# Kernel optimization log

Hardware: AMD Instinct MI355X
Metric: run time of the kernel (lower is better)

## Reference

```python
import jax, jax.numpy as jnp
import numpy as np

B, L, D_MODEL, N_HEADS = 2, 2048, 1024, 16
RANK = max(N_HEADS, int(D_MODEL * 0.25))            # 256
RANK_PER_HEAD = RANK // N_HEADS                      # 16
HEAD_DIM = D_MODEL // N_HEADS                        # 64


def _rope_cos_sin(L, head_dim, dtype=jnp.float32):
    half = head_dim // 2
    theta = 1.0 / (10000.0 ** (jnp.arange(half, dtype=dtype) / half))
    angles = jnp.arange(L, dtype=dtype)[:, None] * theta[None, :]   # [L, half]
    return jnp.cos(angles), jnp.sin(angles)


def _apply_rope(x, cos, sin):
    # x: [B, L, H, D]; pairs (even, odd) rotated by per-position angle.
    B, L, H, D = x.shape
    xp = x.reshape(B, L, H, D // 2, 2)
    x0, x1 = xp[..., 0], xp[..., 1]
    c = cos[None, :, None, :]
    s = sin[None, :, None, :]
    r0 = x0 * c - x1 * s
    r1 = x0 * s + x1 * c
    return jnp.stack([r0, r1], axis=-1).reshape(B, L, H, D)


def setup_inputs() -> dict:
    key = jax.random.key(0)
    ks = jax.random.split(key, 7)
    x = jax.random.normal(ks[0], (B, L, D_MODEL), dtype=jnp.float32)
    mask = jax.random.randint(ks[1], (B, L), 0, 2, dtype=jnp.int32)
    scale = 0.02
    Wq = jax.random.normal(ks[2], (RANK, D_MODEL), dtype=jnp.float32) * scale
    Wk = jax.random.normal(ks[3], (RANK, D_MODEL), dtype=jnp.float32) * scale
    Wv = jax.random.normal(ks[4], (RANK, D_MODEL), dtype=jnp.float32) * scale
    xav_u = float(np.sqrt(6.0 / (HEAD_DIM + RANK_PER_HEAD)))
    U = jax.random.uniform(ks[5], (N_HEADS, HEAD_DIM, RANK_PER_HEAD), dtype=jnp.float32, minval=-xav_u, maxval=xav_u)
    V = jax.random.uniform(ks[6], (N_HEADS, RANK_PER_HEAD, HEAD_DIM), dtype=jnp.float32, minval=-xav_u, maxval=xav_u)
    return {"x": x, "Wq": Wq, "Wk": Wk, "Wv": Wv, "U": U, "V": V, "mask": mask}


def reference(x, Wq, Wk, Wv, U, V, mask):
    Bq, Lq, _ = x.shape
    H, HD, RH = U.shape
    q_low = (x @ Wq.T).reshape(Bq, Lq, H, RH)
    k_low = (x @ Wk.T).reshape(Bq, Lq, H, RH)
    v_low = (x @ Wv.T).reshape(Bq, Lq, H, RH)
    # up-project q/k to head_dim via shared U
    q = jnp.einsum('hdr,blhr->blhd', U, q_low)
    k = jnp.einsum('hdr,blhr->blhd', U, k_low)
    cos, sin = _rope_cos_sin(Lq, HD, x.dtype)
    q = _apply_rope(q, cos, sin)
    k = _apply_rope(k, cos, sin)
    attn = jnp.einsum('blhd,bmhd->bhlm', q, k) / jnp.sqrt(jnp.asarray(HD, x.dtype))
    key_mask = mask.astype(bool)[:, None, None, :]           # [B,1,1,M]
    attn = jnp.where(key_mask, attn, jnp.asarray(-jnp.inf, attn.dtype))
    attn = jax.nn.softmax(attn, axis=-1)
    out = jnp.einsum('bhlm,bmhr->blhr', attn, v_low)
    out = jnp.einsum('blhr,hrd->blhd', out, V)
    return out.reshape(Bq, Lq, H * HD)
```

## Files before the change

kernel.cpp:

```cpp
#include <hip/hip_runtime.h>
#include <hip/hip_bf16.h>

typedef unsigned short u16;
typedef unsigned int u32;
typedef __bf16 bf16x8 __attribute__((ext_vector_type(8)));
typedef float f32x4 __attribute__((ext_vector_type(4)));

#define NB 2
#define NL 2048
#define NDM 1024
#define NH 16
#define NHD 64
#define NRH 16
#define NCOL 2304

#define QSCL 0.18033688011112042f

#define AS1(p) ((const __attribute__((address_space(1))) void*)(p))
#define AS3(p) ((__attribute__((address_space(3))) void*)(p))

__device__ __forceinline__ u16 f2bf(float f) {
  u32 u = __builtin_bit_cast(u32, f);
  u32 r = (u + 0x7fffu + ((u >> 16) & 1u)) >> 16;
  return (u16)r;
}

__global__ void k_prep_weff(const float* __restrict__ Wq, const float* __restrict__ Wk,
                            const float* __restrict__ Wv, const float* __restrict__ U,
                            u16* __restrict__ Wall) {
  int idx = blockIdx.x * 256 + threadIdx.x;
  int col = idx & 1023;
  int row = idx >> 10;
  float acc;
  if (row < 2048) {
    const float* W = (row < 1024) ? Wq : Wk;
    int rr = row & 1023;
    int h = rr >> 6, d = rr & 63;
    const float* Uh = U + (h * NHD + d) * NRH;
    const float* Wr = W + (size_t)(h * NRH) * NDM + col;
    acc = 0.f;
#pragma unroll
    for (int r = 0; r < 16; ++r) acc += Uh[r] * Wr[(size_t)r * NDM];
  } else {
    acc = Wv[(size_t)(row - 2048) * NDM + col];
  }
  Wall[idx] = f2bf(acc);
}

__global__ void k_cast_x(const float* __restrict__ x, u16* __restrict__ xb) {
  int i = blockIdx.x * 256 + threadIdx.x;
  float2 v = *(const float2*)(x + (size_t)i * 2);
  ushort2 o;
  o.x = f2bf(v.x);
  o.y = f2bf(v.y);
  *(ushort2*)(xb + (size_t)i * 2) = o;
}

__global__ void k_cstab(float2* __restrict__ cstab) {
  int i = blockIdx.x * 256 + threadIdx.x;
  if (i >= NL * 32) return;
  int l = i >> 5, j = i & 31;
  float theta = 1.0f / powf(10000.0f, (float)j * (1.0f / 32.0f));
  float ang = (float)l * theta;
  cstab[i] = float2{cosf(ang), sinf(ang)};
}

__global__ void k_fbias(const int* __restrict__ mask, float* __restrict__ fb) {
  int i = blockIdx.x * 256 + threadIdx.x;
  fb[i] = mask[i] ? 0.f : -1e30f;
}

__global__ __launch_bounds__(256) void k_gemm(const u16* __restrict__ A,
                                              const u16* __restrict__ Bm,
                                              const float2* __restrict__ cstab,
                                              u16* __restrict__ qt,
                                              u16* __restrict__ ktb,
                                              u16* __restrict__ vT) {
  __shared__ char lds[32768];
  const int tid = threadIdx.x;
  const int wave = tid >> 6, lane = tid & 63;
  const int bm = blockIdx.x, bn = blockIdx.y;
  const int wr = wave >> 1, wc = wave & 1;
  const char* Ag = (const char*)(A + (size_t)bm * 128 * NDM);
  const char* Bg = (const char*)(Bm + (size_t)bn * 128 * NDM);
  f32x4 acc[4][4] = {};
  for (int kt = 0; kt < 16; ++kt) {
    __syncthreads();
#pragma unroll
    for (int i = 0; i < 4; ++i) {
      int off = wave * 4096 + i * 1024 + lane * 16;
      int src = off ^ ((off >> 3) & 0x70);
      int ga = (src >> 7) * 2048 + kt * 128 + (src & 127);
      __builtin_amdgcn_global_load_lds(AS1(Ag + ga), AS3(lds + wave * 4096 + i * 1024), 16, 0, 0);
      __builtin_amdgcn_global_load_lds(AS1(Bg + ga), AS3(lds + 16384 + wave * 4096 + i * 1024), 16, 0, 0);
    }
    __syncthreads();
#pragma unroll
    for (int kk = 0; kk < 2; ++kk) {
      bf16x8 af[4], bfr[4];
#pragma unroll
      for (int m = 0; m < 4; ++m) {
        int row = wr * 64 + m * 16 + (lane & 15);
        int byte = row * 128 + kk * 64 + ((lane >> 4) << 4);
        af[m] = *(const bf16x8*)(lds + (byte ^ ((row & 7) << 4)));
      }
#pragma unroll
      for (int n = 0; n < 4; ++n) {
        int row = wc * 64 + n * 16 + (lane & 15);
        int byte = row * 128 + kk * 64 + ((lane >> 4) << 4);
        bfr[n] = *(const bf16x8*)(lds + 16384 + (byte ^ ((row & 7) << 4)));
      }
#pragma unroll
      for (int m = 0; m < 4; ++m)
#pragma unroll
        for (int n = 0; n < 4; ++n)
          acc[m][n] = __builtin_amdgcn_mfma_f32_16x16x32_bf16(af[m], bfr[n], acc[m][n], 0, 0, 0);
    }
  }

  const int r0 = bm * 128 + wr * 64;
  const int b = r0 >> 11;
  if (bn < 16) {
    const bool isq = (bn < 8);
    u16* dst = isq ? qt : ktb;
    const float qs = isq ? QSCL : 1.0f;
    const int hh = (isq ? bn : bn - 8) * 2 + wc;
    const int par = lane & 1;
    const size_t base = ((size_t)(b * NH + hh)) * NL;
#pragma unroll
    for (int n = 0; n < 4; ++n) {
      const int d = n * 16 + (lane & 15);
      const int j = d >> 1;
#pragma unroll
      for (int m = 0; m < 4; ++m) {
#pragma unroll
        for (int r = 0; r < 4; ++r) {
          int row = r0 + m * 16 + ((lane >> 4) << 2) + r;
          int l = row & 2047;
          float2 cs = cstab[l * 32 + j];
          float v = acc[m][n][r];
          float pv = __shfl_xor(v, 1);
          float ov = par ? (pv * cs.y + v * cs.x) : (v * cs.x - pv * cs.y);
          dst[((base + l) << 6) + d] = f2bf(ov * qs);
        }
      }
    }
  } else {
    const int rr = lane & 15;
#pragma unroll
    for (int n = 0; n < 4; ++n) {
      const int hh = (bn - 16) * 8 + wc * 4 + n;
      const size_t vbase = ((size_t)(b * NH + hh) * NRH + rr) * NL;
#pragma unroll
      for (int m = 0; m < 4; ++m) {
        int row0 = r0 + m * 16 + ((lane >> 4) << 2);
        int l = row0 & 2047;
        int l6 = l & 63;
        int P = (l & ~63) | (((l6 >> 4) & 1) << 5) | (((l6 >> 5) & 1) << 2) |
                (((l6 >> 2) & 3) << 3) | (l6 & 3);
        ushort4 o4;
        o4.x = f2bf(acc[m][n][0]);
        o4.y = f2bf(acc[m][n][1]);
        o4.z = f2bf(acc[m][n][2]);
        o4.w = f2bf(acc[m][n][3]);
        *(ushort4*)(vT + vbase + P) = o4;
      }
    }
  }
}

__global__ __launch_bounds__(256) void k_attn(const u16* __restrict__ qt,
                                              const u16* __restrict__ ktp,
                                              const u16* __restrict__ vT,
                                              const float* __restrict__ fbias,
                                              float* __restrict__ Oattn) {
  __shared__ char lds[16384];
  const int tid = threadIdx.x, wave = tid >> 6, lane = tid & 63;
  int blk = (int)blockIdx.x;
  blk = (blk & 7) * 128 + (blk >> 3);
  const int qtile = blk & 31, h = (blk >> 5) & 15, b = blk >> 9;
  const size_t bh = (size_t)(b * NH + h);
  const u16* Q = qt + (bh * NL + (size_t)qtile * 64) * 64;
  const u16* K = ktp + bh * NL * 64;
  const u16* Vt = vT + bh * NRH * NL;
  const float* fbb = fbias + b * NL;

  const int g = lane >> 4, qi = lane & 15;
  const int swq = (qi & 7) << 4;

  const int qr = wave * 16 + qi;
  bf16x8 qf0 = *(const bf16x8*)(Q + qr * 64 + g * 8);
  bf16x8 qf1 = *(const bf16x8*)(Q + qr * 64 + 32 + g * 8);

  f32x4 o = {0.f, 0.f, 0.f, 0.f};
  float Ls = 0.f;

  const u16* Vrow = Vt + (size_t)qi * NL + g * 8;
  const float* fbg = fbb + g * 4;
  int koff[4][2];
#pragma unroll
  for (int n = 0; n < 4; ++n)
#pragma unroll
    for (int dc = 0; dc < 2; ++dc)
      koff[n][dc] = (((n * 16 + qi) * 128 + dc * 64 + g * 16) ^ swq);

#pragma unroll
  for (int i = 0; i < 2; ++i) {
    int off = wave * 2048 + i * 1024 + lane * 16;
    int src = off ^ ((off >> 3) & 0x70);
    __builtin_amdgcn_global_load_lds(AS1((const char*)K + src),
                                     AS3(lds + wave * 2048 + i * 1024), 16, 0, 0);
  }
  f32x4 cfb0 = *(const f32x4*)(fbg);
  f32x4 cfb1 = *(const f32x4*)(fbg + 16);
  f32x4 cfb2 = *(const f32x4*)(fbg + 32);
  f32x4 cfb3 = *(const f32x4*)(fbg + 48);
  bf16x8 cvf0 = *(const bf16x8*)(Vrow);
  bf16x8 cvf1 = *(const bf16x8*)(Vrow + 32);

  int cur = 0;
  for (int t = 0; t < 32; ++t) {
    __syncthreads();
    f32x4 nfb0 = {}, nfb1 = {}, nfb2 = {}, nfb3 = {};
    bf16x8 nvf0 = {}, nvf1 = {};
    if (t < 31) {
      const char* Kg = (const char*)(K + (size_t)(t + 1) * 4096);
      char* Kn = lds + (cur ^ 1) * 8192;
#pragma unroll
      for (int i = 0; i < 2; ++i) {
        int off = wave * 2048 + i * 1024 + lane * 16;
        int src = off ^ ((off >> 3) & 0x70);
        __builtin_amdgcn_global_load_lds(AS1(Kg + src),
                                         AS3(Kn + wave * 2048 + i * 1024), 16, 0, 0);
      }
      const float* fbt = fbg + (t + 1) * 64;
      nfb0 = *(const f32x4*)(fbt);
      nfb1 = *(const f32x4*)(fbt + 16);
      nfb2 = *(const f32x4*)(fbt + 32);
      nfb3 = *(const f32x4*)(fbt + 48);
      const u16* Vtt = Vrow + (t + 1) * 64;
      nvf0 = *(const bf16x8*)(Vtt);
      nvf1 = *(const bf16x8*)(Vtt + 32);
    }
    const char* Kcur = lds + cur * 8192;

    f32x4 s0, s1, s2, s3;
#define QK(n, dst, fbv)                                                    \
  {                                                                        \
    bf16x8 k0 = *(const bf16x8*)(Kcur + koff[n][0]);                       \
    bf16x8 k1 = *(const bf16x8*)(Kcur + koff[n][1]);                       \
    f32x4 z = __builtin_amdgcn_mfma_f32_16x16x32_bf16(k0, qf0, fbv, 0, 0, 0); \
    dst = __builtin_amdgcn_mfma_f32_16x16x32_bf16(k1, qf1, z, 0, 0, 0);    \
  }
    QK(0, s0, cfb0) QK(1, s1, cfb1) QK(2, s2, cfb2) QK(3, s3, cfb3)
#undef QK

    float p00 = __builtin_amdgcn_exp2f(s0[0]), p01 = __builtin_amdgcn_exp2f(s0[1]);
    float p02 = __builtin_amdgcn_exp2f(s0[2]), p03 = __builtin_amdgcn_exp2f(s0[3]);
    float p10 = __builtin_amdgcn_exp2f(s1[0]), p11 = __builtin_amdgcn_exp2f(s1[1]);
    float p12 = __builtin_amdgcn_exp2f(s1[2]), p13 = __builtin_amdgcn_exp2f(s1[3]);
    float p20 = __builtin_amdgcn_exp2f(s2[0]), p21 = __builtin_amdgcn_exp2f(s2[1]);
    float p22 = __builtin_amdgcn_exp2f(s2[2]), p23 = __builtin_amdgcn_exp2f(s2[3]);
    float p30 = __builtin_amdgcn_exp2f(s3[0]), p31 = __builtin_amdgcn_exp2f(s3[1]);
    float p32 = __builtin_amdgcn_exp2f(s3[2]), p33 = __builtin_amdgcn_exp2f(s3[3]);
    float rs = (((p00 + p01) + (p02 + p03)) + ((p10 + p11) + (p12 + p13))) +
               (((p20 + p21) + (p22 + p23)) + ((p30 + p31) + (p32 + p33)));
    Ls += rs;

    bf16x8 pf0, pf1;
    pf0[0] = (__bf16)p00; pf0[1] = (__bf16)p01; pf0[2] = (__bf16)p02; pf0[3] = (__bf16)p03;
    pf0[4] = (__bf16)p20; pf0[5] = (__bf16)p21; pf0[6] = (__bf16)p22; pf0[7] = (__bf16)p23;
    pf1[0] = (__bf16)p10; pf1[1] = (__bf16)p11; pf1[2] = (__bf16)p12; pf1[3] = (__bf16)p13;
    pf1[4] = (__bf16)p30; pf1[5] = (__bf16)p31; pf1[6] = (__bf16)p32; pf1[7] = (__bf16)p33;

    o = __builtin_amdgcn_mfma_f32_16x16x32_bf16(pf0, cvf0, o, 0, 0, 0);
    o = __builtin_amdgcn_mfma_f32_16x16x32_bf16(pf1, cvf1, o, 0, 0, 0);

    cfb0 = nfb0; cfb1 = nfb1; cfb2 = nfb2; cfb3 = nfb3;
    cvf0 = nvf0; cvf1 = nvf1;
    cur ^= 1;
  }

  Ls += __shfl_xor(Ls, 16);
  Ls += __shfl_xor(Ls, 32);
  const size_t qrow0 = bh * NL + (size_t)qtile * 64 + wave * 16;
#pragma unroll
  for (int i = 0; i < 4; ++i) {
    float Li = __shfl(Ls, g * 4 + i);
    Oattn[(qrow0 + g * 4 + i) * NRH + qi] = o[i] / Li;
  }
}

__global__ void k_proj(const float* __restrict__ Oattn, const float* __restrict__ V,
                       float* __restrict__ out) {
  int bl = blockIdx.x;
  int b = bl >> 11, l = bl & 2047;
  __shared__ float sO[256];
  int tid = threadIdx.x;
  sO[tid] = Oattn[((size_t)(b * NH + (tid >> 4)) * NL + l) * NRH + (tid & 15)];
  __syncthreads();
#pragma unroll
  for (int p = 0; p < 4; ++p) {
    int h = (tid >> 6) + p * 4;
    int d = tid & 63;
    float acc = 0.f;
    const float* Vh = V + (size_t)(h * NRH) * NHD + d;
    const float* Oh = sO + h * NRH;
#pragma unroll
    for (int r = 0; r < 16; ++r) acc += Oh[r] * Vh[(size_t)r * NHD];
    out[(size_t)bl * NDM + h * NHD + d] = acc;
  }
}

extern "C" void kernel_launch(void* const* d_in, const int* in_sizes, int n_in,
                              void* d_out, int out_size, void* d_ws, size_t ws_size,
                              hipStream_t stream) {
  (void)in_sizes; (void)n_in; (void)out_size; (void)ws_size;
  const float* x  = (const float*)d_in[0];
  const float* Wq = (const float*)d_in[1];
  const float* Wk = (const float*)d_in[2];
  const float* Wv = (const float*)d_in[3];
  const float* U  = (const float*)d_in[4];
  const float* Vm = (const float*)d_in[5];
  const int* mask = (const int*)d_in[6];
  float* out = (float*)d_out;
  char* ws = (char*)d_ws;

  u16* Wall     = (u16*)(ws);
  u16* xb       = (u16*)(ws + 4718592);
  float* Oattn  = (float*)(ws + 13107200);
  float* fbias  = (float*)(ws + 17301504);
  u16* qt       = (u16*)(ws + 31981568);
  u16* ktb      = (u16*)(ws + 40370176);
  u16* vT       = (u16*)(ws + 48758784);
  float2* cstab = (float2*)(ws + 50855936);

  k_prep_weff<<<dim3(9216), dim3(256), 0, stream>>>(Wq, Wk, Wv, U, Wall);
  k_cast_x<<<dim3(8192), dim3(256), 0, stream>>>(x, xb);
  k_cstab<<<dim3(256), dim3(256), 0, stream>>>(cstab);
  k_fbias<<<dim3(16), dim3(256), 0, stream>>>(mask, fbias);
  k_gemm<<<dim3(32, 18), dim3(256), 0, stream>>>(xb, Wall, cstab, qt, ktb, vT);
  k_attn<<<dim3(1024), dim3(256), 0, stream>>>(qt, ktb, vT, fbias, Oattn);
  k_proj<<<dim3(4096), dim3(256), 0, stream>>>(Oattn, Vm, out);
}
```

Baseline: 133.7 us.

## Load K fragments directly from global into registers, dropping LDS staging

The attention kernel previously staged each 64-key K tile into double-buffered LDS with global_load_lds and a __syncthreads per iteration, then read swizzled fragments back. Now each wave loads its K MFMA fragments straight from global memory into registers, prefetching the next tile one iteration ahead, and the LDS buffer and block barrier are removed. This removes the barrier and the LDS round trip, but each of the 4 waves now fetches the full K tile separately (4x redundant global/L2 traffic) and register pressure rises.

```diff
diff --git a/kernel.cpp b/kernel.cpp
--- a/kernel.cpp
+++ b/kernel.cpp
@@ -174,7 +174,6 @@
                                               const u16* __restrict__ vT,
                                               const float* __restrict__ fbias,
                                               float* __restrict__ Oattn) {
-  __shared__ char lds[16384];
   const int tid = threadIdx.x, wave = tid >> 6, lane = tid & 63;
   int blk = (int)blockIdx.x;
   blk = (blk & 7) * 128 + (blk >> 3);
@@ -186,7 +185,6 @@
   const float* fbb = fbias + b * NL;
 
   const int g = lane >> 4, qi = lane & 15;
-  const int swq = (qi & 7) << 4;
 
   const int qr = wave * 16 + qi;
   bf16x8 qf0 = *(const bf16x8*)(Q + qr * 64 + g * 8);
@@ -195,65 +193,58 @@
   f32x4 o = {0.f, 0.f, 0.f, 0.f};
   float Ls = 0.f;
 
+  const u16* Krow = K + (size_t)qi * 64 + g * 8;
   const u16* Vrow = Vt + (size_t)qi * NL + g * 8;
   const float* fbg = fbb + g * 4;
-  int koff[4][2];
-#pragma unroll
-  for (int n = 0; n < 4; ++n)
-#pragma unroll
-    for (int dc = 0; dc < 2; ++dc)
-      koff[n][dc] = (((n * 16 + qi) * 128 + dc * 64 + g * 16) ^ swq);
-
-#pragma unroll
-  for (int i = 0; i < 2; ++i) {
-    int off = wave * 2048 + i * 1024 + lane * 16;
-    int src = off ^ ((off >> 3) & 0x70);
-    __builtin_amdgcn_global_load_lds(AS1((const char*)K + src),
-                                     AS3(lds + wave * 2048 + i * 1024), 16, 0, 0);
-  }
+
+  bf16x8 ck0 = *(const bf16x8*)(Krow);
+  bf16x8 ck1 = *(const bf16x8*)(Krow + 32);
+  bf16x8 ck2 = *(const bf16x8*)(Krow + 1024);
+  bf16x8 ck3 = *(const bf16x8*)(Krow + 1024 + 32);
+  bf16x8 ck4 = *(const bf16x8*)(Krow + 2048);
+  bf16x8 ck5 = *(const bf16x8*)(Krow + 2048 + 32);
+  bf16x8 ck6 = *(const bf16x8*)(Krow + 3072);
+  bf16x8 ck7 = *(const bf16x8*)(Krow + 3072 + 32);
   f32x4 cfb0 = *(const f32x4*)(fbg);
   f32x4 cfb1 = *(const f32x4*)(fbg + 16);
   f32x4 cfb2 = *(const f32x4*)(fbg + 32);
   f32x4 cfb3 = *(const f32x4*)(fbg + 48);
-  bf16x8 cvf0 = *(const bf16x8*)(Vrow);
-  bf16x8 cvf1 = *(const bf16x8*)(Vrow + 32);
-
-  int cur = 0;
+  bf16x8 cv0 = *(const bf16x8*)(Vrow);
+  bf16x8 cv1 = *(const bf16x8*)(Vrow + 32);
+
   for (int t = 0; t < 32; ++t) {
-    __syncthreads();
+    bf16x8 nk0 = {}, nk1 = {}, nk2 = {}, nk3 = {}, nk4 = {}, nk5 = {}, nk6 = {}, nk7 = {};
     f32x4 nfb0 = {}, nfb1 = {}, nfb2 = {}, nfb3 = {};
-    bf16x8 nvf0 = {}, nvf1 = {};
+    bf16x8 nv0 = {}, nv1 = {};
     if (t < 31) {
-      const char* Kg = (const char*)(K + (size_t)(t + 1) * 4096);
-      char* Kn = lds + (cur ^ 1) * 8192;
-#pragma unroll
-      for (int i = 0; i < 2; ++i) {
-        int off = wave * 2048 + i * 1024 + lane * 16;
-        int src = off ^ ((off >> 3) & 0x70);
-        __builtin_amdgcn_global_load_lds(AS1(Kg + src),
-                                         AS3(Kn + wave * 2048 + i * 1024), 16, 0, 0);
-      }
+      const u16* Kt = Krow + (t + 1) * 4096;
+      nk0 = *(const bf16x8*)(Kt);
+      nk1 = *(const bf16x8*)(Kt + 32);
+      nk2 = *(const bf16x8*)(Kt + 1024);
+      nk3 = *(const bf16x8*)(Kt + 1024 + 32);
+      nk4 = *(const bf16x8*)(Kt + 2048);
+      nk5 = *(const bf16x8*)(Kt + 2048 + 32);
+      nk6 = *(const bf16x8*)(Kt + 3072);
+      nk7 = *(const bf16x8*)(Kt + 3072 + 32);
       const float* fbt = fbg + (t + 1) * 64;
       nfb0 = *(const f32x4*)(fbt);
       nfb1 = *(const f32x4*)(fbt + 16);
       nfb2 = *(const f32x4*)(fbt + 32);
       nfb3 = *(const f32x4*)(fbt + 48);
       const u16* Vtt = Vrow + (t + 1) * 64;
-      nvf0 = *(const bf16x8*)(Vtt);
-      nvf1 = *(const bf16x8*)(Vtt + 32);
-    }
-    const char* Kcur = lds + cur * 8192;
+      nv0 = *(const bf16x8*)(Vtt);
+      nv1 = *(const bf16x8*)(Vtt + 32);
+    }
 
     f32x4 s0, s1, s2, s3;
-#define QK(n, dst, fbv)                                                    \
-  {                                                                        \
-    bf16x8 k0 = *(const bf16x8*)(Kcur + koff[n][0]);                       \
-    bf16x8 k1 = *(const bf16x8*)(Kcur + koff[n][1]);                       \
-    f32x4 z = __builtin_amdgcn_mfma_f32_16x16x32_bf16(k0, qf0, fbv, 0, 0, 0); \
-    dst = __builtin_amdgcn_mfma_f32_16x16x32_bf16(k1, qf1, z, 0, 0, 0);    \
-  }
-    QK(0, s0, cfb0) QK(1, s1, cfb1) QK(2, s2, cfb2) QK(3, s3, cfb3)
-#undef QK
+    s0 = __builtin_amdgcn_mfma_f32_16x16x32_bf16(ck0, qf0, cfb0, 0, 0, 0);
+    s0 = __builtin_amdgcn_mfma_f32_16x16x32_bf16(ck1, qf1, s0, 0, 0, 0);
+    s1 = __builtin_amdgcn_mfma_f32_16x16x32_bf16(ck2, qf0, cfb1, 0, 0, 0);
+    s1 = __builtin_amdgcn_mfma_f32_16x16x32_bf16(ck3, qf1, s1, 0, 0, 0);
+    s2 = __builtin_amdgcn_mfma_f32_16x16x32_bf16(ck4, qf0, cfb2, 0, 0, 0);
+    s2 = __builtin_amdgcn_mfma_f32_16x16x32_bf16(ck5, qf1, s2, 0, 0, 0);
+    s3 = __builtin_amdgcn_mfma_f32_16x16x32_bf16(ck6, qf0, cfb3, 0, 0, 0);
+    s3 = __builtin_amdgcn_mfma_f32_16x16x32_bf16(ck7, qf1, s3, 0, 0, 0);
 
     float p00 = __builtin_amdgcn_exp2f(s0[0]), p01 = __builtin_amdgcn_exp2f(s0[1]);
     float p02 = __builtin_amdgcn_exp2f(s0[2]), p03 = __builtin_amdgcn_exp2f(s0[3]);
@@ -273,12 +264,13 @@
     pf1[0] = (__bf16)p10; pf1[1] = (__bf16)p11; pf1[2] = (__bf16)p12; pf1[3] = (__bf16)p13;
     pf1[4] = (__bf16)p30; pf1[5] = (__bf16)p31; pf1[6] = (__bf16)p32; pf1[7] = (__bf16)p33;
 
-    o = __builtin_amdgcn_mfma_f32_16x16x32_bf16(pf0, cvf0, o, 0, 0, 0);
-    o = __builtin_amdgcn_mfma_f32_16x16x32_bf16(pf1, cvf1, o, 0, 0, 0);
-
+    o = __builtin_amdgcn_mfma_f32_16x16x32_bf16(pf0, cv0, o, 0, 0, 0);
+    o = __builtin_amdgcn_mfma_f32_16x16x32_bf16(pf1, cv1, o, 0, 0, 0);
+
+    ck0 = nk0; ck1 = nk1; ck2 = nk2; ck3 = nk3;
+    ck4 = nk4; ck5 = nk5; ck6 = nk6; ck7 = nk7;
     cfb0 = nfb0; cfb1 = nfb1; cfb2 = nfb2; cfb3 = nfb3;
-    cvf0 = nvf0; cvf1 = nvf1;
-    cur ^= 1;
+    cv0 = nv0; cv1 = nv1;
   }
 
   Ls += __shfl_xor(Ls, 16);
```

Result: slower. 234.2 us (+75.2%).
